# Kernel tuning notes

Measured on AMD Instinct MI355X. Metric: run time of the kernel, lower is better.

Reference implementation:

```python
import jax, jax.numpy as jnp
import numpy as np

H = 1024
NH = 16
HD = H // NH
EPS = 1e-5


def setup_inputs() -> dict:
    key = jax.random.key(0)
    ks = jax.random.split(key, 12)
    B, S = 4, 2048
    scale = 1.0 / np.sqrt(H)
    inp = {
        "x": jax.random.normal(ks[0], (B, S, H), jnp.float32),
        "mask": jnp.ones((B, S), jnp.int32),
        "Wq": jax.random.normal(ks[1], (H, H), jnp.float32) * scale,
        "bq": jnp.zeros((H,), jnp.float32),
        "Wk": jax.random.normal(ks[2], (H, H), jnp.float32) * scale,
        "bk": jnp.zeros((H,), jnp.float32),
        "Wv": jax.random.normal(ks[3], (H, H), jnp.float32) * scale,
        "bv": jnp.zeros((H,), jnp.float32),
        "Wo": jax.random.normal(ks[4], (H, H), jnp.float32) * scale,
        "bo": jnp.zeros((H,), jnp.float32),
        "gamma": jnp.ones((H,), jnp.float32),
        "beta": jnp.zeros((H,), jnp.float32),
    }
    return inp


def reference(x, mask, Wq, bq, Wk, bk, Wv, bv, Wo, bo, gamma, beta):
    B, S, _ = x.shape
    # QKV projections -> [B, NH, S, HD]
    def split_heads(t):
        return t.reshape(B, S, NH, HD).transpose(0, 2, 1, 3)
    q = split_heads(x @ Wq.T + bq)
    k = split_heads(x @ Wk.T + bk)
    v = split_heads(x @ Wv.T + bv)
    # scaled dot-product scores [B, NH, S, S]
    scores = jnp.einsum("bhqd,bhkd->bhqk", q, k) / np.sqrt(HD).astype(np.float32)
    m = (mask[:, None, None, :] == 0)  # [B,1,1,S]
    scores = jnp.where(m, -1e9, scores)
    attn = jax.nn.softmax(scores, axis=-1)
    # dropout is identity at eval time
    attended = jnp.einsum("bhqk,bhkd->bhqd", attn, v)
    attended = attended.transpose(0, 2, 1, 3).reshape(B, S, H)
    out = attended @ Wo.T + bo
    # residual + LayerNorm
    y = x + out
    mu = jnp.mean(y, axis=-1, keepdims=True)
    var = jnp.mean(jnp.square(y - mu), axis=-1, keepdims=True)
    return (y - mu) * jax.lax.rsqrt(var + EPS) * gamma + beta
```

## Files before the change

kernel.cpp:

```cpp
#include <hip/hip_runtime.h>
#include <stdint.h>

#define HDIM 1024
#define NHEAD 16
#define HD 64
#define NB 4
#define SEQ 2048
#define NROWS (NB*SEQ)
#define NBH (NB*NHEAD)

typedef __attribute__((ext_vector_type(8))) short short8;
typedef __attribute__((ext_vector_type(4))) float f32x4;

typedef __attribute__((address_space(1))) const void gk_t;
typedef __attribute__((address_space(3))) void lds_t;

static __device__ __forceinline__ unsigned short f2bf(float f) {
  union { float f; unsigned u; } v; v.f = f;
  unsigned r = v.u + 0x7fffu + ((v.u >> 16) & 1u);
  return (unsigned short)(r >> 16);
}

__global__ __launch_bounds__(256) void cvt_f32_bf16(const float* __restrict__ in,
                                                    unsigned short* __restrict__ out,
                                                    int n4) {
  int i = blockIdx.x * 256 + threadIdx.x;
  if (i >= n4) return;
  float4 v = reinterpret_cast<const float4*>(in)[i];
  ushort4 o;
  o.x = f2bf(v.x); o.y = f2bf(v.y); o.z = f2bf(v.z); o.w = f2bf(v.w);
  reinterpret_cast<ushort4*>(out)[i] = o;
}

__global__ __launch_bounds__(256) void cvt_weights(
    const float* __restrict__ Wq, const float* __restrict__ Wk,
    const float* __restrict__ Wv, const float* __restrict__ Wo,
    unsigned short* __restrict__ wqkv, unsigned short* __restrict__ wo) {
  int which = blockIdx.x >> 10;
  int i = (blockIdx.x & 1023) * 256 + threadIdx.x;
  const float* src = (which == 0) ? Wq : (which == 1) ? Wk : (which == 2) ? Wv : Wo;
  unsigned short* dst = (which < 3) ? (wqkv + (size_t)which * 1048576) : wo;
  float4 v = reinterpret_cast<const float4*>(src)[i];
  ushort4 o;
  o.x = f2bf(v.x); o.y = f2bf(v.y); o.z = f2bf(v.z); o.w = f2bf(v.w);
  reinterpret_cast<ushort4*>(dst)[i] = o;
}

__global__ __launch_bounds__(256) void mask_prep(const int* __restrict__ mask,
                                                 float* __restrict__ fb,
                                                 unsigned* __restrict__ flags) {
  if (blockIdx.x < 32) {
    int i = blockIdx.x * 256 + threadIdx.x;
    fb[i] = (mask[i] == 0) ? -1e9f : 0.0f;
  } else {
    int i = threadIdx.x;
    __shared__ unsigned char sh[128];
    if (i < 128) {
      int b = i >> 5, t = i & 31;
      const int* mrow = mask + b * SEQ + t * 64;
      int any = 0;
#pragma unroll 8
      for (int j = 0; j < 64; ++j) any |= (mrow[j] == 0);
      sh[i] = (unsigned char)any;
    }
    __syncthreads();
    if (i < NB) {
      unsigned f = 0;
      for (int t2 = 0; t2 < 32; ++t2) f |= (sh[i * 32 + t2] ? 1u : 0u) << t2;
      flags[i] = f;
    }
  }
}

static __device__ __forceinline__ void gemm_mainloop256(
    const unsigned short* __restrict__ A, const unsigned short* __restrict__ B,
    int rowA0, int rowB0,
    char* As , char* Bs ,
    f32x4 acc[4][4]) {
  const int tid  = threadIdx.x;
  const int lane = tid & 63;
  const int wave = tid >> 6;
  const int l15 = lane & 15, g = lane >> 4;
  const int wm = wave >> 1, wn = wave & 1;
  const int srow8 = lane >> 3;
  const int schunk = lane & 7;

  const int wbase = wave * 1024;

#define STAGE_TILE(buf, kt)                                                        \
  {                                                                                \
    _Pragma("unroll")                                                              \
    for (int a = 0; a < 4; ++a) {                                                  \
      int row = a * 64 + wave * 8 + srow8;                                         \
      int chunk = schunk ^ (row & 7);                                              \
      const unsigned short* ga = A + (size_t)(rowA0 + row) * 1024 + (kt) + chunk * 8; \
      __builtin_amdgcn_global_load_lds((gk_t*)ga,                                  \
          (lds_t*)(As + (buf) * 32768 + a * 8192 + wbase), 16, 0, 0);              \
    }                                                                              \
    _Pragma("unroll")                                                              \
    for (int a = 0; a < 2; ++a) {                                                  \
      int row = a * 64 + wave * 8 + srow8;                                         \
      int chunk = schunk ^ (row & 7);                                              \
      const unsigned short* gb = B + (size_t)(rowB0 + row) * 1024 + (kt) + chunk * 8; \
      __builtin_amdgcn_global_load_lds((gk_t*)gb,                                  \
          (lds_t*)(Bs + (buf) * 16384 + a * 8192 + wbase), 16, 0, 0);              \
    }                                                                              \
  }

  STAGE_TILE(0, 0);
  STAGE_TILE(1, 64);
  STAGE_TILE(2, 128);

#pragma unroll
  for (int t = 0; t < 16; ++t) {
    if (t <= 13)      asm volatile("s_waitcnt vmcnt(12)" ::: "memory");
    else if (t == 14) asm volatile("s_waitcnt vmcnt(6)" ::: "memory");
    else              asm volatile("s_waitcnt vmcnt(0)" ::: "memory");
    __builtin_amdgcn_s_barrier();
    __builtin_amdgcn_sched_barrier(0);

    const char* Ab = As + (t % 3) * 32768;
    const char* Bb = Bs + (t % 3) * 16384;
    short8 af[2][4], bfr[2][4];
#pragma unroll
    for (int ks = 0; ks < 2; ++ks)
#pragma unroll
      for (int mi = 0; mi < 4; ++mi) {
        int row = wm * 64 + mi * 16 + l15;
        af[ks][mi] = *reinterpret_cast<const short8*>(
            Ab + row * 128 + (((ks * 4 + g) ^ (row & 7)) << 4));
      }
#pragma unroll
    for (int ks = 0; ks < 2; ++ks)
#pragma unroll
      for (int ni = 0; ni < 4; ++ni) {
        int row = wn * 64 + ni * 16 + l15;
        bfr[ks][ni] = *reinterpret_cast<const short8*>(
            Bb + row * 128 + (((ks * 4 + g) ^ (row & 7)) << 4));
      }
    asm volatile("s_waitcnt lgkmcnt(0)" ::: "memory");
    __builtin_amdgcn_sched_barrier(0);
    __builtin_amdgcn_s_barrier();
    __builtin_amdgcn_sched_barrier(0);

    if (t + 3 < 16) STAGE_TILE((t + 3) % 3, (t + 3) * 64);
    __builtin_amdgcn_sched_barrier(0);

    __builtin_amdgcn_s_setprio(1);
#pragma unroll
    for (int ks = 0; ks < 2; ++ks)
#pragma unroll
      for (int mi = 0; mi < 4; ++mi)
#pragma unroll
        for (int ni = 0; ni < 4; ++ni)
          acc[mi][ni] = __builtin_amdgcn_mfma_f32_16x16x32_bf16(
              af[ks][mi], bfr[ks][ni], acc[mi][ni], 0, 0, 0);
    __builtin_amdgcn_s_setprio(0);
  }
#undef STAGE_TILE
}

__global__ __launch_bounds__(512) void gemm_qkv(
    const unsigned short* __restrict__ xb, const unsigned short* __restrict__ wqkv,
    const float* __restrict__ bq, const float* __restrict__ bk, const float* __restrict__ bv,
    unsigned short* __restrict__ qout, unsigned short* __restrict__ kout,
    unsigned short* __restrict__ vtout) {
  __shared__ __align__(16) char As[3 * 32768];
  __shared__ __align__(16) char Bs[3 * 16384];
  f32x4 acc[4][4];
  const f32x4 zero = {0.f, 0.f, 0.f, 0.f};
#pragma unroll
  for (int i = 0; i < 4; ++i)
#pragma unroll
    for (int j = 0; j < 4; ++j) acc[i][j] = zero;

  int flat = blockIdx.y * 24 + blockIdx.x;
  int s = (flat & 7) * 96 + (flat >> 3);
  int by = s / 24, bx = s - by * 24;
  const int bm0 = by * 256;
  const int bn0 = bx * 128;
  gemm_mainloop256(xb, wqkv, bm0, bn0, As, Bs, acc);

  const int lane = threadIdx.x & 63, wave = threadIdx.x >> 6;
  const int l15 = lane & 15, g = lane >> 4;
  const int wm = wave >> 1, wn = wave & 1;
#pragma unroll
  for (int mi = 0; mi < 4; ++mi) {
    int m0 = bm0 + wm * 64 + mi * 16 + g * 4;
#pragma unroll
    for (int ni = 0; ni < 4; ++ni) {
      int n = bn0 + wn * 64 + ni * 16 + l15;
      int which = n >> 10;
      int nc = n & 1023;
      float bias = (which == 0 ? bq : which == 1 ? bk : bv)[nc];
      int h = nc >> 6, d = nc & 63;
#pragma unroll
      for (int r = 0; r < 4; ++r) {
        int m = m0 + r;
        int b = m >> 11, ss = m & 2047;
        float v = acc[mi][ni][r] + bias;
        if (which == 0) v *= 0.18033688011112042f;
        unsigned short val = f2bf(v);
        int bh = b * NHEAD + h;
        if (which == 2) {
          vtout[(((size_t)bh * HD + d) << 11) + ss] = val;
        } else {
          unsigned short* dst = (which == 0) ? qout : kout;
          dst[(((size_t)bh << 11) + ss) * HD + d] = val;
        }
      }
    }
  }
}

__global__ __launch_bounds__(512) void gemm_proj(
    const unsigned short* __restrict__ ab, const unsigned short* __restrict__ wob,
    const float* __restrict__ bo, const float* __restrict__ x, float* __restrict__ y) {
  __shared__ __align__(16) char As[3 * 32768];
  __shared__ __align__(16) char Bs[3 * 16384];
  f32x4 acc[4][4];
  const f32x4 zero = {0.f, 0.f, 0.f, 0.f};
#pragma unroll
  for (int i = 0; i < 4; ++i)
#pragma unroll
    for (int j = 0; j < 4; ++j) acc[i][j] = zero;

  int flat = blockIdx.y * 8 + blockIdx.x;
  int s = (flat & 7) * 32 + (flat >> 3);
  int by = s >> 3, bx = s & 7;
  const int bm0 = by * 256;
  const int bn0 = bx * 128;
  gemm_mainloop256(ab, wob, bm0, bn0, As, Bs, acc);

  const int lane = threadIdx.x & 63, wave = threadIdx.x >> 6;
  const int l15 = lane & 15, g = lane >> 4;
  const int wm = wave >> 1, wn = wave & 1;
#pragma unroll
  for (int mi = 0; mi < 4; ++mi) {
    int m0 = bm0 + wm * 64 + mi * 16 + g * 4;
#pragma unroll
    for (int ni = 0; ni < 4; ++ni) {
      int n = bn0 + wn * 64 + ni * 16 + l15;
      float bias = bo[n];
#pragma unroll
      for (int r = 0; r < 4; ++r) {
        size_t idx = (size_t)(m0 + r) * HDIM + n;
        y[idx] = acc[mi][ni][r] + bias + x[idx];
      }
    }
  }
}

__global__ __launch_bounds__(512) void flash_attn(
    const unsigned short* __restrict__ Q, const unsigned short* __restrict__ K,
    const unsigned short* __restrict__ VT, const float* __restrict__ fbias,
    const unsigned* __restrict__ mflagsPtr,
    unsigned short* __restrict__ O) {
  __shared__ __align__(16) char Ks[2][64 * 128];
  __shared__ __align__(16) char Vs[2][64 * 128];
  __shared__ __align__(16) char Ps[8 * 16 * 128];

  const int tid = threadIdx.x;
  const int lane = tid & 63, wave = tid >> 6;
  const int l15 = lane & 15, g = lane >> 4;
  const int bh = blockIdx.y;
  const int b = bh >> 4, h = bh & 15;
  const int q0 = blockIdx.x * 128;

  const unsigned short* qptr = Q + ((size_t)bh * SEQ + q0 + wave * 16 + l15) * HD + g * 8;
  short8 qf0 = *reinterpret_cast<const short8*>(qptr);
  short8 qf1 = *reinterpret_cast<const short8*>(qptr + 32);

  const f32x4 zero = {0.f, 0.f, 0.f, 0.f};
  f32x4 oacc[4];
#pragma unroll
  for (int i = 0; i < 4; ++i) oacc[i] = zero;
  f32x4 lacc = zero;
  const unsigned mflags = mflagsPtr[b];

  short8 ones;
#pragma unroll
  for (int i = 0; i < 8; ++i) ones[i] = (short)0x3F80;

  const int srow = tid >> 3;
  const int scol = (tid & 7) << 3;
  const int swzs = (srow & 7) << 4;
  const int stoff = srow * 128 + ((scol * 2) ^ swzs);
  char* kd0 = Ks[0] + stoff; char* kd1 = Ks[1] + stoff;
  char* vd0 = Vs[0] + stoff; char* vd1 = Vs[1] + stoff;
  const unsigned short* kg = K + ((size_t)bh * SEQ + srow) * HD + scol;
  const unsigned short* vg = VT + (((size_t)bh * HD + srow) << 11) + scol;

  const int cfrag = g << 4;
  const int swzr = (l15 & 7) << 4;
  const float* fbrow = fbias + b * SEQ;
  char* prow = Ps + wave * 2048 + l15 * 128;

  short8 kp = *reinterpret_cast<const short8*>(kg);
  short8 vp = *reinterpret_cast<const short8*>(vg);
  *reinterpret_cast<short8*>(kd0) = kp;
  *reinterpret_cast<short8*>(vd0) = vp;
  kp = *reinterpret_cast<const short8*>(kg + (size_t)64 * HD);
  vp = *reinterpret_cast<const short8*>(vg + 64);
  __syncthreads();

  auto step = [&](int jt, const char* Kr, const char* Vr, char* Kw, char* Vw) {
    f32x4 sf[4];
    __builtin_amdgcn_s_setprio(1);
#pragma unroll
    for (int ni = 0; ni < 4; ++ni) {
      const char* kr = Kr + (ni * 16 + l15) * 128;
      short8 a0 = *reinterpret_cast<const short8*>(kr + (cfrag ^ swzr));
      short8 a1 = *reinterpret_cast<const short8*>(kr + ((cfrag + 64) ^ swzr));
      f32x4 t = __builtin_amdgcn_mfma_f32_16x16x32_bf16(a0, qf0, zero, 0, 0, 0);
      sf[ni] = __builtin_amdgcn_mfma_f32_16x16x32_bf16(a1, qf1, t, 0, 0, 0);
    }
    __builtin_amdgcn_s_setprio(0);

    if (jt + 1 < SEQ / 64) {
      *reinterpret_cast<short8*>(Kw) = kp;
      *reinterpret_cast<short8*>(Vw) = vp;
    }

    if (__builtin_amdgcn_readfirstlane((mflags >> jt) & 1u)) {
#pragma unroll
      for (int ni = 0; ni < 4; ++ni) {
        f32x4 fbv = *reinterpret_cast<const f32x4*>(fbrow + jt * 64 + ni * 16 + 4 * g);
#pragma unroll
        for (int r = 0; r < 4; ++r) sf[ni][r] += fbv[r];
      }
    }

#pragma unroll
    for (int ni = 0; ni < 4; ++ni)
#pragma unroll
      for (int r = 0; r < 4; ++r)
        sf[ni][r] = __builtin_amdgcn_exp2f(sf[ni][r]);

#pragma unroll
    for (int ni = 0; ni < 4; ++ni) {
      unsigned lo_, hi_;
      asm("v_cvt_pk_bf16_f32 %0, %1, %2" : "=v"(lo_) : "v"(sf[ni][0]), "v"(sf[ni][1]));
      asm("v_cvt_pk_bf16_f32 %0, %1, %2" : "=v"(hi_) : "v"(sf[ni][2]), "v"(sf[ni][3]));
      *reinterpret_cast<uint2*>(prow + ((32 * ni + 8 * g) ^ swzr)) = make_uint2(lo_, hi_);
    }
    asm volatile("s_waitcnt lgkmcnt(0)" ::: "memory");
    __builtin_amdgcn_sched_barrier(0);
    short8 pb0 = *reinterpret_cast<const short8*>(prow + (cfrag ^ swzr));
    short8 pb1 = *reinterpret_cast<const short8*>(prow + ((cfrag + 64) ^ swzr));

    __builtin_amdgcn_s_setprio(1);
#pragma unroll
    for (int di = 0; di < 4; ++di) {
      const char* vr = Vr + (di * 16 + l15) * 128;
      short8 va0 = *reinterpret_cast<const short8*>(vr + (cfrag ^ swzr));
      short8 va1 = *reinterpret_cast<const short8*>(vr + ((cfrag + 64) ^ swzr));
      oacc[di] = __builtin_amdgcn_mfma_f32_16x16x32_bf16(va0, pb0, oacc[di], 0, 0, 0);
      oacc[di] = __builtin_amdgcn_mfma_f32_16x16x32_bf16(va1, pb1, oacc[di], 0, 0, 0);
    }
    lacc = __builtin_amdgcn_mfma_f32_16x16x32_bf16(ones, pb0, lacc, 0, 0, 0);
    lacc = __builtin_amdgcn_mfma_f32_16x16x32_bf16(ones, pb1, lacc, 0, 0, 0);
    __builtin_amdgcn_s_setprio(0);

    if (jt + 2 < SEQ / 64) {
      kp = *reinterpret_cast<const short8*>(kg + (size_t)(jt + 2) * 64 * HD);
      vp = *reinterpret_cast<const short8*>(vg + (jt + 2) * 64);
    }
  };

  for (int jt = 0; jt < SEQ / 64; jt += 2) {
    step(jt,     Ks[0], Vs[0], kd1, vd1);
    __syncthreads();
    step(jt + 1, Ks[1], Vs[1], kd0, vd0);
    __syncthreads();
  }

  {
    float inv = 1.0f / lacc[0];
    char* orow_lds = Ps + (wave * 16 + l15) * 128;
#pragma unroll
    for (int di = 0; di < 4; ++di) {
      float e0 = oacc[di][0] * inv, e1 = oacc[di][1] * inv;
      float e2 = oacc[di][2] * inv, e3 = oacc[di][3] * inv;
      unsigned lo_, hi_;
      asm("v_cvt_pk_bf16_f32 %0, %1, %2" : "=v"(lo_) : "v"(e0), "v"(e1));
      asm("v_cvt_pk_bf16_f32 %0, %1, %2" : "=v"(hi_) : "v"(e2), "v"(e3));
      char* dst = orow_lds + ((32 * di + 8 * g) ^ swzr);
      *reinterpret_cast<uint2*>(dst) = make_uint2(lo_, hi_);
    }
  }
  __syncthreads();
  {
    int q = tid >> 2;
    int c4 = tid & 3;
    int swz = (q & 7) << 4;
    const char* src = Ps + q * 128;
    short8 o0 = *reinterpret_cast<const short8*>(src + ((c4 * 32) ^ swz));
    short8 o1 = *reinterpret_cast<const short8*>(src + ((c4 * 32 + 16) ^ swz));
    unsigned short* orow = O + ((size_t)b * SEQ + q0 + q) * HDIM + h * 64 + c4 * 16;
    *reinterpret_cast<short8*>(orow) = o0;
    *reinterpret_cast<short8*>(orow + 8) = o1;
  }
}

__global__ __launch_bounds__(256) void layernorm(float* __restrict__ y,
                                                 const float* __restrict__ gamma,
                                                 const float* __restrict__ beta) {
  const int row = blockIdx.x;
  float* yr = y + (size_t)row * HDIM;
  const int tid = threadIdx.x;
  float4 v = reinterpret_cast<const float4*>(yr)[tid];
  float s = v.x + v.y + v.z + v.w;
  float s2 = v.x * v.x + v.y * v.y + v.z * v.z + v.w * v.w;
#pragma unroll
  for (int off = 1; off < 64; off <<= 1) {
    s += __shfl_xor(s, off);
    s2 += __shfl_xor(s2, off);
  }
  __shared__ float red[8];
  const int wave = tid >> 6, lane = tid & 63;
  if (lane == 0) { red[wave] = s; red[wave + 4] = s2; }
  __syncthreads();
  s = red[0] + red[1] + red[2] + red[3];
  s2 = red[4] + red[5] + red[6] + red[7];
  float mean = s * (1.f / HDIM);
  float var = s2 * (1.f / HDIM) - mean * mean;
  float rstd = rsqrtf(var + 1e-5f);
  float4 g = reinterpret_cast<const float4*>(gamma)[tid];
  float4 bt = reinterpret_cast<const float4*>(beta)[tid];
  float4 o;
  o.x = (v.x - mean) * rstd * g.x + bt.x;
  o.y = (v.y - mean) * rstd * g.y + bt.y;
  o.z = (v.z - mean) * rstd * g.z + bt.z;
  o.w = (v.w - mean) * rstd * g.w + bt.w;
  reinterpret_cast<float4*>(yr)[tid] = o;
}

extern "C" void kernel_launch(void* const* d_in, const int* in_sizes, int n_in,
                              void* d_out, int out_size, void* d_ws, size_t ws_size,
                              hipStream_t stream) {
  (void)in_sizes; (void)n_in; (void)out_size; (void)ws_size;
  const float* x     = (const float*)d_in[0];
  const int*   mask  = (const int*)d_in[1];
  const float* Wq    = (const float*)d_in[2];
  const float* bq    = (const float*)d_in[3];
  const float* Wk    = (const float*)d_in[4];
  const float* bk    = (const float*)d_in[5];
  const float* Wv    = (const float*)d_in[6];
  const float* bv    = (const float*)d_in[7];
  const float* Wo    = (const float*)d_in[8];
  const float* bo    = (const float*)d_in[9];
  const float* gamma = (const float*)d_in[10];
  const float* beta  = (const float*)d_in[11];
  float* out = (float*)d_out;

  char* ws = (char*)d_ws;
  unsigned short* xb   = (unsigned short*)(ws);
  unsigned short* wqkv = (unsigned short*)(ws + 16777216);
  unsigned short* wo   = (unsigned short*)(ws + 16777216 + 6291456);
  unsigned short* q    = (unsigned short*)(ws + 25165824);
  unsigned short* k    = (unsigned short*)(ws + 25165824 + 16777216);
  unsigned short* vt   = (unsigned short*)(ws + 25165824 + 2 * 16777216);
  unsigned short* attn = xb;
  float* fbias = (float*)(ws + 16777216);
  unsigned* mflags = (unsigned*)(ws + 16777216 + NB * SEQ * 4);

  cvt_f32_bf16<<<8192, 256, 0, stream>>>(x, xb, NROWS * HDIM / 4);
  cvt_weights<<<4096, 256, 0, stream>>>(Wq, Wk, Wv, Wo, wqkv, wo);

  gemm_qkv<<<dim3(24, 32), 512, 0, stream>>>(xb, wqkv, bq, bk, bv, q, k, vt);
  mask_prep<<<33, 256, 0, stream>>>(mask, fbias, mflags);
  flash_attn<<<dim3(16, 64), 512, 0, stream>>>(q, k, vt, fbias, mflags, attn);
  gemm_proj<<<dim3(8, 32), 512, 0, stream>>>(attn, wo, bo, x, out);
  layernorm<<<NROWS, 256, 0, stream>>>(out, gamma, beta);
}
```

Before: 219.1 us.

## Retile projection GEMMs to 128-row tiles with double buffering and two blocks per CU

Both projection GEMMs move from 256x128 tiles with a triple-buffered LDS pipeline to 128-row tiles (384 or 256 columns wide) with a double-buffered pipeline. The waves are rearranged 2x4, and launch bounds request two blocks per CU. The aim is to cut LDS use so two blocks can run per CU, and to balance the wave count across CUs (512 and 256 blocks). The trade-off is a shallower prefetch, since each step waits with vmcnt(0) for the next tile, so load latency is hidden less and the grouped block swizzle for L2 reuse is dropped.

```diff
diff --git a/kernel.cpp b/kernel.cpp
--- a/kernel.cpp
+++ b/kernel.cpp
@@ -72,58 +72,59 @@
   }
 }
 
-static __device__ __forceinline__ void gemm_mainloop256(
+template<int NI>
+static __device__ __forceinline__ void gemm_mainloop_v2(
     const unsigned short* __restrict__ A, const unsigned short* __restrict__ B,
     int rowA0, int rowB0,
     char* As , char* Bs ,
-    f32x4 acc[4][4]) {
+    f32x4 acc[4][NI]) {
   const int tid  = threadIdx.x;
   const int lane = tid & 63;
   const int wave = tid >> 6;
   const int l15 = lane & 15, g = lane >> 4;
-  const int wm = wave >> 1, wn = wave & 1;
+  const int wm = wave >> 2, wn = wave & 3;
   const int srow8 = lane >> 3;
   const int schunk = lane & 7;
-
   const int wbase = wave * 1024;
-
-#define STAGE_TILE(buf, kt)                                                        \
+  const int BBUF = NI * 8192;
+
+#define STAGE_V2(buf, kt)                                                          \
   {                                                                                \
     _Pragma("unroll")                                                              \
-    for (int a = 0; a < 4; ++a) {                                                  \
+    for (int a = 0; a < 2; ++a) {                                                  \
       int row = a * 64 + wave * 8 + srow8;                                         \
       int chunk = schunk ^ (row & 7);                                              \
       const unsigned short* ga = A + (size_t)(rowA0 + row) * 1024 + (kt) + chunk * 8; \
       __builtin_amdgcn_global_load_lds((gk_t*)ga,                                  \
-          (lds_t*)(As + (buf) * 32768 + a * 8192 + wbase), 16, 0, 0);              \
+          (lds_t*)(As + (buf) * 16384 + a * 8192 + wbase), 16, 0, 0);              \
     }                                                                              \
     _Pragma("unroll")                                                              \
-    for (int a = 0; a < 2; ++a) {                                                  \
+    for (int a = 0; a < NI; ++a) {                                                 \
       int row = a * 64 + wave * 8 + srow8;                                         \
       int chunk = schunk ^ (row & 7);                                              \
       const unsigned short* gb = B + (size_t)(rowB0 + row) * 1024 + (kt) + chunk * 8; \
       __builtin_amdgcn_global_load_lds((gk_t*)gb,                                  \
-          (lds_t*)(Bs + (buf) * 16384 + a * 8192 + wbase), 16, 0, 0);              \
+          (lds_t*)(Bs + (buf) * BBUF + a * 8192 + wbase), 16, 0, 0);               \
     }                                                                              \
   }
 
-  STAGE_TILE(0, 0);
-  STAGE_TILE(1, 64);
-  STAGE_TILE(2, 128);
+  STAGE_V2(0, 0);
 
 #pragma unroll
   for (int t = 0; t < 16; ++t) {
-    if (t <= 13)      asm volatile("s_waitcnt vmcnt(12)" ::: "memory");
-    else if (t == 14) asm volatile("s_waitcnt vmcnt(6)" ::: "memory");
-    else              asm volatile("s_waitcnt vmcnt(0)" ::: "memory");
+    asm volatile("s_waitcnt vmcnt(0)" ::: "memory");
+    __builtin_amdgcn_sched_barrier(0);
     __builtin_amdgcn_s_barrier();
     __builtin_amdgcn_sched_barrier(0);
 
-    const char* Ab = As + (t % 3) * 32768;
-    const char* Bb = Bs + (t % 3) * 16384;
-    short8 af[2][4], bfr[2][4];
-#pragma unroll
-    for (int ks = 0; ks < 2; ++ks)
+    if (t + 1 < 16) STAGE_V2((t + 1) & 1, (t + 1) * 64);
+    __builtin_amdgcn_sched_barrier(0);
+
+    const char* Ab = As + (t & 1) * 16384;
+    const char* Bb = Bs + (t & 1) * BBUF;
+    short8 af[2][4], bfr[2][NI];
+#pragma unroll
+    for (int ks = 0; ks < 2; ++ks) {
 #pragma unroll
       for (int mi = 0; mi < 4; ++mi) {
         int row = wm * 64 + mi * 16 + l15;
@@ -131,20 +132,14 @@
             Ab + row * 128 + (((ks * 4 + g) ^ (row & 7)) << 4));
       }
 #pragma unroll
-    for (int ks = 0; ks < 2; ++ks)
-#pragma unroll
-      for (int ni = 0; ni < 4; ++ni) {
-        int row = wn * 64 + ni * 16 + l15;
+      for (int ni = 0; ni < NI; ++ni) {
+        int row = wn * (NI * 16) + ni * 16 + l15;
         bfr[ks][ni] = *reinterpret_cast<const short8*>(
             Bb + row * 128 + (((ks * 4 + g) ^ (row & 7)) << 4));
       }
+    }
     asm volatile("s_waitcnt lgkmcnt(0)" ::: "memory");
     __builtin_amdgcn_sched_barrier(0);
-    __builtin_amdgcn_s_barrier();
-    __builtin_amdgcn_sched_barrier(0);
-
-    if (t + 3 < 16) STAGE_TILE((t + 3) % 3, (t + 3) * 64);
-    __builtin_amdgcn_sched_barrier(0);
 
     __builtin_amdgcn_s_setprio(1);
 #pragma unroll
@@ -152,44 +147,43 @@
 #pragma unroll
       for (int mi = 0; mi < 4; ++mi)
 #pragma unroll
-        for (int ni = 0; ni < 4; ++ni)
+        for (int ni = 0; ni < NI; ++ni)
           acc[mi][ni] = __builtin_amdgcn_mfma_f32_16x16x32_bf16(
               af[ks][mi], bfr[ks][ni], acc[mi][ni], 0, 0, 0);
     __builtin_amdgcn_s_setprio(0);
   }
-#undef STAGE_TILE
-}
-
-__global__ __launch_bounds__(512) void gemm_qkv(
+#undef STAGE_V2
+}
+
+__global__ __launch_bounds__(512, 2) void gemm_qkv(
     const unsigned short* __restrict__ xb, const unsigned short* __restrict__ wqkv,
     const float* __restrict__ bq, const float* __restrict__ bk, const float* __restrict__ bv,
     unsigned short* __restrict__ qout, unsigned short* __restrict__ kout,
     unsigned short* __restrict__ vtout) {
-  __shared__ __align__(16) char As[3 * 32768];
-  __shared__ __align__(16) char Bs[3 * 16384];
-  f32x4 acc[4][4];
+  __shared__ __align__(16) char As[2 * 16384];
+  __shared__ __align__(16) char Bs[2 * 6 * 8192];
+  f32x4 acc[4][6];
   const f32x4 zero = {0.f, 0.f, 0.f, 0.f};
 #pragma unroll
   for (int i = 0; i < 4; ++i)
 #pragma unroll
-    for (int j = 0; j < 4; ++j) acc[i][j] = zero;
-
-  int flat = blockIdx.y * 24 + blockIdx.x;
-  int s = (flat & 7) * 96 + (flat >> 3);
-  int by = s / 24, bx = s - by * 24;
-  const int bm0 = by * 256;
-  const int bn0 = bx * 128;
-  gemm_mainloop256(xb, wqkv, bm0, bn0, As, Bs, acc);
+    for (int j = 0; j < 6; ++j) acc[i][j] = zero;
+
+  const int flat = blockIdx.x;
+  const int bx = flat & 7, by = flat >> 3;
+  const int bm0 = by * 128;
+  const int bn0 = bx * 384;
+  gemm_mainloop_v2<6>(xb, wqkv, bm0, bn0, As, Bs, acc);
 
   const int lane = threadIdx.x & 63, wave = threadIdx.x >> 6;
   const int l15 = lane & 15, g = lane >> 4;
-  const int wm = wave >> 1, wn = wave & 1;
+  const int wm = wave >> 2, wn = wave & 3;
 #pragma unroll
   for (int mi = 0; mi < 4; ++mi) {
     int m0 = bm0 + wm * 64 + mi * 16 + g * 4;
 #pragma unroll
-    for (int ni = 0; ni < 4; ++ni) {
-      int n = bn0 + wn * 64 + ni * 16 + l15;
+    for (int ni = 0; ni < 6; ++ni) {
+      int n = bn0 + wn * 96 + ni * 16 + l15;
       int which = n >> 10;
       int nc = n & 1023;
       float bias = (which == 0 ? bq : which == 1 ? bk : bv)[nc];
@@ -213,11 +207,11 @@
   }
 }
 
-__global__ __launch_bounds__(512) void gemm_proj(
+__global__ __launch_bounds__(512, 2) void gemm_proj(
     const unsigned short* __restrict__ ab, const unsigned short* __restrict__ wob,
     const float* __restrict__ bo, const float* __restrict__ x, float* __restrict__ y) {
-  __shared__ __align__(16) char As[3 * 32768];
-  __shared__ __align__(16) char Bs[3 * 16384];
+  __shared__ __align__(16) char As[2 * 16384];
+  __shared__ __align__(16) char Bs[2 * 4 * 8192];
   f32x4 acc[4][4];
   const f32x4 zero = {0.f, 0.f, 0.f, 0.f};
 #pragma unroll
@@ -225,16 +219,15 @@
 #pragma unroll
     for (int j = 0; j < 4; ++j) acc[i][j] = zero;
 
-  int flat = blockIdx.y * 8 + blockIdx.x;
-  int s = (flat & 7) * 32 + (flat >> 3);
-  int by = s >> 3, bx = s & 7;
-  const int bm0 = by * 256;
-  const int bn0 = bx * 128;
-  gemm_mainloop256(ab, wob, bm0, bn0, As, Bs, acc);
+  const int flat = blockIdx.x;
+  const int bx = flat & 3, by = flat >> 2;
+  const int bm0 = by * 128;
+  const int bn0 = bx * 256;
+  gemm_mainloop_v2<4>(ab, wob, bm0, bn0, As, Bs, acc);
 
   const int lane = threadIdx.x & 63, wave = threadIdx.x >> 6;
   const int l15 = lane & 15, g = lane >> 4;
-  const int wm = wave >> 1, wn = wave & 1;
+  const int wm = wave >> 2, wn = wave & 3;
 #pragma unroll
   for (int mi = 0; mi < 4; ++mi) {
     int m0 = bm0 + wm * 64 + mi * 16 + g * 4;
@@ -468,9 +461,9 @@
   cvt_f32_bf16<<<8192, 256, 0, stream>>>(x, xb, NROWS * HDIM / 4);
   cvt_weights<<<4096, 256, 0, stream>>>(Wq, Wk, Wv, Wo, wqkv, wo);
 
-  gemm_qkv<<<dim3(24, 32), 512, 0, stream>>>(xb, wqkv, bq, bk, bv, q, k, vt);
+  gemm_qkv<<<512, 512, 0, stream>>>(xb, wqkv, bq, bk, bv, q, k, vt);
   mask_prep<<<33, 256, 0, stream>>>(mask, fbias, mflags);
   flash_attn<<<dim3(16, 64), 512, 0, stream>>>(q, k, vt, fbias, mflags, attn);
-  gemm_proj<<<dim3(8, 32), 512, 0, stream>>>(attn, wo, bo, x, out);
+  gemm_proj<<<256, 512, 0, stream>>>(attn, wo, bo, x, out);
   layernorm<<<NROWS, 256, 0, stream>>>(out, gamma, beta);
 }
```

Result: slower. 241.9 us (+10.4%).

## Process two 16-row query groups per wave in flash attention

Applied to the files above, without the earlier changes.

Each wave now handles 32 query rows instead of 16, so a block covers 256 queries and the grid halves. Each K and V fragment read from LDS and each K/V tile staged from global memory is reused across twice as many queries, cutting LDS and global K/V traffic per unit of work. The cost is more registers per wave (double accumulators and score tiles), a larger P buffer in LDS, and only 512 blocks, which may lower occupancy and leave fewer blocks to spread across the GPU.

```diff
diff --git a/kernel.cpp b/kernel.cpp
--- a/kernel.cpp
+++ b/kernel.cpp
@@ -84,7 +84,6 @@
   const int wm = wave >> 1, wn = wave & 1;
   const int srow8 = lane >> 3;
   const int schunk = lane & 7;
-
   const int wbase = wave * 1024;
 
 #define STAGE_TILE(buf, kt)                                                        \
@@ -258,24 +257,29 @@
     unsigned short* __restrict__ O) {
   __shared__ __align__(16) char Ks[2][64 * 128];
   __shared__ __align__(16) char Vs[2][64 * 128];
-  __shared__ __align__(16) char Ps[8 * 16 * 128];
+  __shared__ __align__(16) char Ps[8 * 32 * 128];
 
   const int tid = threadIdx.x;
   const int lane = tid & 63, wave = tid >> 6;
   const int l15 = lane & 15, g = lane >> 4;
   const int bh = blockIdx.y;
   const int b = bh >> 4, h = bh & 15;
-  const int q0 = blockIdx.x * 128;
-
-  const unsigned short* qptr = Q + ((size_t)bh * SEQ + q0 + wave * 16 + l15) * HD + g * 8;
-  short8 qf0 = *reinterpret_cast<const short8*>(qptr);
-  short8 qf1 = *reinterpret_cast<const short8*>(qptr + 32);
+  const int q0 = blockIdx.x * 256;
+
+  const unsigned short* qptr =
+      Q + ((size_t)bh * SEQ + q0 + wave * 32 + l15) * HD + g * 8;
+  short8 qfa0 = *reinterpret_cast<const short8*>(qptr);
+  short8 qfa1 = *reinterpret_cast<const short8*>(qptr + 32);
+  short8 qfb0 = *reinterpret_cast<const short8*>(qptr + 16 * HD);
+  short8 qfb1 = *reinterpret_cast<const short8*>(qptr + 16 * HD + 32);
 
   const f32x4 zero = {0.f, 0.f, 0.f, 0.f};
-  f32x4 oacc[4];
-#pragma unroll
-  for (int i = 0; i < 4; ++i) oacc[i] = zero;
-  f32x4 lacc = zero;
+  f32x4 oacc[2][4];
+#pragma unroll
+  for (int qg = 0; qg < 2; ++qg)
+#pragma unroll
+    for (int i = 0; i < 4; ++i) oacc[qg][i] = zero;
+  f32x4 lacc0 = zero, lacc1 = zero;
   const unsigned mflags = mflagsPtr[b];
 
   short8 ones;
@@ -294,7 +298,8 @@
   const int cfrag = g << 4;
   const int swzr = (l15 & 7) << 4;
   const float* fbrow = fbias + b * SEQ;
-  char* prow = Ps + wave * 2048 + l15 * 128;
+  char* prow0 = Ps + wave * 4096 + l15 * 128;
+  char* prow1 = prow0 + 2048;
 
   short8 kp = *reinterpret_cast<const short8*>(kg);
   short8 vp = *reinterpret_cast<const short8*>(vg);
@@ -305,15 +310,17 @@
   __syncthreads();
 
   auto step = [&](int jt, const char* Kr, const char* Vr, char* Kw, char* Vw) {
-    f32x4 sf[4];
+    f32x4 sf[2][4];
     __builtin_amdgcn_s_setprio(1);
 #pragma unroll
     for (int ni = 0; ni < 4; ++ni) {
       const char* kr = Kr + (ni * 16 + l15) * 128;
       short8 a0 = *reinterpret_cast<const short8*>(kr + (cfrag ^ swzr));
       short8 a1 = *reinterpret_cast<const short8*>(kr + ((cfrag + 64) ^ swzr));
-      f32x4 t = __builtin_amdgcn_mfma_f32_16x16x32_bf16(a0, qf0, zero, 0, 0, 0);
-      sf[ni] = __builtin_amdgcn_mfma_f32_16x16x32_bf16(a1, qf1, t, 0, 0, 0);
+      f32x4 t0 = __builtin_amdgcn_mfma_f32_16x16x32_bf16(a0, qfa0, zero, 0, 0, 0);
+      sf[0][ni] = __builtin_amdgcn_mfma_f32_16x16x32_bf16(a1, qfa1, t0, 0, 0, 0);
+      f32x4 t1 = __builtin_amdgcn_mfma_f32_16x16x32_bf16(a0, qfb0, zero, 0, 0, 0);
+      sf[1][ni] = __builtin_amdgcn_mfma_f32_16x16x32_bf16(a1, qfb1, t1, 0, 0, 0);
     }
     __builtin_amdgcn_s_setprio(0);
 
@@ -327,27 +334,34 @@
       for (int ni = 0; ni < 4; ++ni) {
         f32x4 fbv = *reinterpret_cast<const f32x4*>(fbrow + jt * 64 + ni * 16 + 4 * g);
 #pragma unroll
-        for (int r = 0; r < 4; ++r) sf[ni][r] += fbv[r];
+        for (int r = 0; r < 4; ++r) { sf[0][ni][r] += fbv[r]; sf[1][ni][r] += fbv[r]; }
       }
     }
 
 #pragma unroll
-    for (int ni = 0; ni < 4; ++ni)
-#pragma unroll
-      for (int r = 0; r < 4; ++r)
-        sf[ni][r] = __builtin_amdgcn_exp2f(sf[ni][r]);
+    for (int qg = 0; qg < 2; ++qg)
+#pragma unroll
+      for (int ni = 0; ni < 4; ++ni)
+#pragma unroll
+        for (int r = 0; r < 4; ++r)
+          sf[qg][ni][r] = __builtin_amdgcn_exp2f(sf[qg][ni][r]);
 
 #pragma unroll
     for (int ni = 0; ni < 4; ++ni) {
-      unsigned lo_, hi_;
-      asm("v_cvt_pk_bf16_f32 %0, %1, %2" : "=v"(lo_) : "v"(sf[ni][0]), "v"(sf[ni][1]));
-      asm("v_cvt_pk_bf16_f32 %0, %1, %2" : "=v"(hi_) : "v"(sf[ni][2]), "v"(sf[ni][3]));
-      *reinterpret_cast<uint2*>(prow + ((32 * ni + 8 * g) ^ swzr)) = make_uint2(lo_, hi_);
+      unsigned lo0, hi0, lo1, hi1;
+      asm("v_cvt_pk_bf16_f32 %0, %1, %2" : "=v"(lo0) : "v"(sf[0][ni][0]), "v"(sf[0][ni][1]));
+      asm("v_cvt_pk_bf16_f32 %0, %1, %2" : "=v"(hi0) : "v"(sf[0][ni][2]), "v"(sf[0][ni][3]));
+      asm("v_cvt_pk_bf16_f32 %0, %1, %2" : "=v"(lo1) : "v"(sf[1][ni][0]), "v"(sf[1][ni][1]));
+      asm("v_cvt_pk_bf16_f32 %0, %1, %2" : "=v"(hi1) : "v"(sf[1][ni][2]), "v"(sf[1][ni][3]));
+      *reinterpret_cast<uint2*>(prow0 + ((32 * ni + 8 * g) ^ swzr)) = make_uint2(lo0, hi0);
+      *reinterpret_cast<uint2*>(prow1 + ((32 * ni + 8 * g) ^ swzr)) = make_uint2(lo1, hi1);
     }
     asm volatile("s_waitcnt lgkmcnt(0)" ::: "memory");
     __builtin_amdgcn_sched_barrier(0);
-    short8 pb0 = *reinterpret_cast<const short8*>(prow + (cfrag ^ swzr));
-    short8 pb1 = *reinterpret_cast<const short8*>(prow + ((cfrag + 64) ^ swzr));
+    short8 pb00 = *reinterpret_cast<const short8*>(prow0 + (cfrag ^ swzr));
+    short8 pb01 = *reinterpret_cast<const short8*>(prow0 + ((cfrag + 64) ^ swzr));
+    short8 pb10 = *reinterpret_cast<const short8*>(prow1 + (cfrag ^ swzr));
+    short8 pb11 = *reinterpret_cast<const short8*>(prow1 + ((cfrag + 64) ^ swzr));
 
     __builtin_amdgcn_s_setprio(1);
 #pragma unroll
@@ -355,11 +369,15 @@
       const char* vr = Vr + (di * 16 + l15) * 128;
       short8 va0 = *reinterpret_cast<const short8*>(vr + (cfrag ^ swzr));
       short8 va1 = *reinterpret_cast<const short8*>(vr + ((cfrag + 64) ^ swzr));
-      oacc[di] = __builtin_amdgcn_mfma_f32_16x16x32_bf16(va0, pb0, oacc[di], 0, 0, 0);
-      oacc[di] = __builtin_amdgcn_mfma_f32_16x16x32_bf16(va1, pb1, oacc[di], 0, 0, 0);
-    }
-    lacc = __builtin_amdgcn_mfma_f32_16x16x32_bf16(ones, pb0, lacc, 0, 0, 0);
-    lacc = __builtin_amdgcn_mfma_f32_16x16x32_bf16(ones, pb1, lacc, 0, 0, 0);
+      oacc[0][di] = __builtin_amdgcn_mfma_f32_16x16x32_bf16(va0, pb00, oacc[0][di], 0, 0, 0);
+      oacc[0][di] = __builtin_amdgcn_mfma_f32_16x16x32_bf16(va1, pb01, oacc[0][di], 0, 0, 0);
+      oacc[1][di] = __builtin_amdgcn_mfma_f32_16x16x32_bf16(va0, pb10, oacc[1][di], 0, 0, 0);
+      oacc[1][di] = __builtin_amdgcn_mfma_f32_16x16x32_bf16(va1, pb11, oacc[1][di], 0, 0, 0);
+    }
+    lacc0 = __builtin_amdgcn_mfma_f32_16x16x32_bf16(ones, pb00, lacc0, 0, 0, 0);
+    lacc0 = __builtin_amdgcn_mfma_f32_16x16x32_bf16(ones, pb01, lacc0, 0, 0, 0);
+    lacc1 = __builtin_amdgcn_mfma_f32_16x16x32_bf16(ones, pb10, lacc1, 0, 0, 0);
+    lacc1 = __builtin_amdgcn_mfma_f32_16x16x32_bf16(ones, pb11, lacc1, 0, 0, 0);
     __builtin_amdgcn_s_setprio(0);
 
     if (jt + 2 < SEQ / 64) {
@@ -376,30 +394,37 @@
   }
 
   {
-    float inv = 1.0f / lacc[0];
-    char* orow_lds = Ps + (wave * 16 + l15) * 128;
-#pragma unroll
-    for (int di = 0; di < 4; ++di) {
-      float e0 = oacc[di][0] * inv, e1 = oacc[di][1] * inv;
-      float e2 = oacc[di][2] * inv, e3 = oacc[di][3] * inv;
-      unsigned lo_, hi_;
-      asm("v_cvt_pk_bf16_f32 %0, %1, %2" : "=v"(lo_) : "v"(e0), "v"(e1));
-      asm("v_cvt_pk_bf16_f32 %0, %1, %2" : "=v"(hi_) : "v"(e2), "v"(e3));
-      char* dst = orow_lds + ((32 * di + 8 * g) ^ swzr);
-      *reinterpret_cast<uint2*>(dst) = make_uint2(lo_, hi_);
+#pragma unroll
+    for (int qg = 0; qg < 2; ++qg) {
+      float inv = 1.0f / (qg == 0 ? lacc0[0] : lacc1[0]);
+      char* orow_lds = Ps + wave * 4096 + (qg * 16 + l15) * 128;
+#pragma unroll
+      for (int di = 0; di < 4; ++di) {
+        float e0 = oacc[qg][di][0] * inv, e1 = oacc[qg][di][1] * inv;
+        float e2 = oacc[qg][di][2] * inv, e3 = oacc[qg][di][3] * inv;
+        unsigned lo_, hi_;
+        asm("v_cvt_pk_bf16_f32 %0, %1, %2" : "=v"(lo_) : "v"(e0), "v"(e1));
+        asm("v_cvt_pk_bf16_f32 %0, %1, %2" : "=v"(hi_) : "v"(e2), "v"(e3));
+        char* dst = orow_lds + ((32 * di + 8 * g) ^ swzr);
+        *reinterpret_cast<uint2*>(dst) = make_uint2(lo_, hi_);
+      }
     }
   }
   __syncthreads();
   {
-    int q = tid >> 2;
-    int c4 = tid & 3;
+    int q = tid >> 1;
+    int hf = tid & 1;
     int swz = (q & 7) << 4;
     const char* src = Ps + q * 128;
-    short8 o0 = *reinterpret_cast<const short8*>(src + ((c4 * 32) ^ swz));
-    short8 o1 = *reinterpret_cast<const short8*>(src + ((c4 * 32 + 16) ^ swz));
-    unsigned short* orow = O + ((size_t)b * SEQ + q0 + q) * HDIM + h * 64 + c4 * 16;
-    *reinterpret_cast<short8*>(orow) = o0;
-    *reinterpret_cast<short8*>(orow + 8) = o1;
+    short8 r0 = *reinterpret_cast<const short8*>(src + ((hf * 64 +  0) ^ swz));
+    short8 r1 = *reinterpret_cast<const short8*>(src + ((hf * 64 + 16) ^ swz));
+    short8 r2 = *reinterpret_cast<const short8*>(src + ((hf * 64 + 32) ^ swz));
+    short8 r3 = *reinterpret_cast<const short8*>(src + ((hf * 64 + 48) ^ swz));
+    unsigned short* orow = O + ((size_t)b * SEQ + q0 + q) * HDIM + h * 64 + hf * 32;
+    reinterpret_cast<short8*>(orow)[0] = r0;
+    reinterpret_cast<short8*>(orow)[1] = r1;
+    reinterpret_cast<short8*>(orow)[2] = r2;
+    reinterpret_cast<short8*>(orow)[3] = r3;
   }
 }
 
@@ -470,7 +495,7 @@
 
   gemm_qkv<<<dim3(24, 32), 512, 0, stream>>>(xb, wqkv, bq, bk, bv, q, k, vt);
   mask_prep<<<33, 256, 0, stream>>>(mask, fbias, mflags);
-  flash_attn<<<dim3(16, 64), 512, 0, stream>>>(q, k, vt, fbias, mflags, attn);
+  flash_attn<<<dim3(8, 64), 512, 0, stream>>>(q, k, vt, fbias, mflags, attn);
   gemm_proj<<<dim3(8, 32), 512, 0, stream>>>(attn, wo, bo, x, out);
   layernorm<<<NROWS, 256, 0, stream>>>(out, gamma, beta);
 }
```

Result: no change. 217.0 us, median of 2 (-1.0%).
